# Performance work log

Measured on AMD Instinct MI355X. Metric: run time of the kernel, lower is better.

## Reference

```python
import jax, jax.numpy as jnp
import numpy as np

N_DETS = 8192
DEG = 64
E = N_DETS * DEG
NUM_BLOCKS = 8
SHORTCUT = 128   # shortcutDim
RED = 32         # reducedDim
INNER = 64       # blockInnerDim = 2*32
PW_RAW = 9
PW_HID = 256
PW_OUT = 32


def setup_inputs() -> dict:
    key = jax.random.key(0)
    ks = jax.random.split(key, 24)
    # valid boxes: x2 > x1, y2 > y1
    x1 = jax.random.uniform(ks[0], (N_DETS, 1), jnp.float32, 0.0, 1000.0)
    y1 = jax.random.uniform(ks[1], (N_DETS, 1), jnp.float32, 0.0, 1000.0)
    w = jax.random.uniform(ks[2], (N_DETS, 1), jnp.float32, 8.0, 128.0)
    h = jax.random.uniform(ks[3], (N_DETS, 1), jnp.float32, 8.0, 128.0)
    dtBoxes = jnp.concatenate([x1, y1, x1 + w, y1 + h], axis=1)
    detScores = jax.random.uniform(ks[4], (N_DETS, 1), jnp.float32)
    # every detection has DEG neighbors (first one is itself) -> no empty segments
    cIdxs = jnp.repeat(jnp.arange(N_DETS, dtype=jnp.int32), DEG)
    nIdxs = jax.random.randint(ks[5], (E,), 0, N_DETS, dtype=jnp.int32)
    nIdxs = nIdxs.at[::DEG].set(jnp.arange(N_DETS, dtype=jnp.int32))
    detFeatures = jnp.zeros((N_DETS, SHORTCUT), jnp.float32)

    def lin(k, fan_in, fan_out):
        b = 1.0 / np.sqrt(fan_in)
        return jax.random.uniform(k, (fan_in, fan_out), jnp.float32, -b, b)

    inp = dict(detScores=detScores, dtBoxes=dtBoxes, detFeatures=detFeatures,
               cIdxs=cIdxs, nIdxs=nIdxs)
    # pairwise feature generator MLP: 9 -> 256 -> 256 -> 32 (ReLU after each)
    inp['pw_W0'] = lin(ks[6], PW_RAW, PW_HID); inp['pw_b0'] = jnp.zeros((PW_HID,), jnp.float32)
    inp['pw_W1'] = lin(ks[7], PW_HID, PW_HID); inp['pw_b1'] = jnp.zeros((PW_HID,), jnp.float32)
    inp['pw_W2'] = lin(ks[8], PW_HID, PW_OUT); inp['pw_b2'] = jnp.zeros((PW_OUT,), jnp.float32)
    # per-block params, stacked over NUM_BLOCKS
    B = NUM_BLOCKS
    inp['blk_fc1_W'] = jnp.stack([lin(jax.random.fold_in(ks[9], i), SHORTCUT, RED) for i in range(B)])
    inp['blk_fc1_b'] = jnp.zeros((B, RED), jnp.float32)
    inp['blk_pw1_W'] = jnp.stack([lin(jax.random.fold_in(ks[10], i), 3 * RED, INNER) for i in range(B)])
    inp['blk_pw1_b'] = jnp.zeros((B, INNER), jnp.float32)
    inp['blk_pw2_W'] = jnp.stack([lin(jax.random.fold_in(ks[11], i), INNER, INNER) for i in range(B)])
    inp['blk_pw2_b'] = jnp.zeros((B, INNER), jnp.float32)
    inp['blk_post_W'] = jnp.stack([jnp.stack([lin(jax.random.fold_in(ks[12], 2 * i + j), INNER, INNER) for j in range(2)]) for i in range(B)])
    inp['blk_post_b'] = jnp.zeros((B, 2, INNER), jnp.float32)
    inp['blk_out_W'] = jnp.stack([lin(jax.random.fold_in(ks[13], i), INNER, SHORTCUT) for i in range(B)])
    inp['blk_out_b'] = jnp.zeros((B, SHORTCUT), jnp.float32)
    return inp


def _pairwise_raw(detScores, dtBoxes, cIdxs, nIdxs):
    # box data (getBoxData)
    x1, y1, x2, y2 = (dtBoxes[:, i:i + 1] for i in range(4))
    w, h = x2 - x1, y2 - y1
    area = w * h
    c, n = cIdxs, nIdxs
    # per-edge IoU (dt_dt_iou gathered at (c,n))
    ix = jnp.maximum(0.0, jnp.minimum(x2[c], x2[n]) - jnp.maximum(x1[c], x1[n]))
    iy = jnp.maximum(0.0, jnp.minimum(y2[c], y2[n]) - jnp.maximum(y1[c], y1[n]))
    inter = ix * iy
    iou = inter / (area[c] + area[n] - inter)
    c_w, c_h, n_w, n_h = w[c], h[c], w[n], h[n]
    c_scale = (c_w + c_h) / 2.0
    c_cx, c_cy = x1[c] + c_w / 2.0, y1[c] + c_h / 2.0
    n_cx, n_cy = x1[n] + n_w / 2.0, y1[n] + n_h / 2.0
    x_dist = n_cx - c_cx
    y_dist = n_cy - c_cy
    l2_dist = jnp.sqrt(x_dist ** 2 + y_dist ** 2) / c_scale
    x_dist = x_dist / c_scale
    y_dist = y_dist / c_scale
    log2 = jnp.log(jnp.float32(2.0))
    w_diff = jnp.log(n_w / c_w) / log2
    h_diff = jnp.log(n_h / c_h) / log2
    aspect_diff = (jnp.log(n_w / n_h) - jnp.log(c_w / c_h)) / log2
    return jnp.concatenate([detScores[c], detScores[n], iou, x_dist, y_dist,
                            l2_dist, w_diff, h_diff, aspect_diff], axis=1)  # [E,9]


def reference(detScores, dtBoxes, detFeatures, pw_W0, pw_b0, pw_W1, pw_b1,
              pw_W2, pw_b2, blk_fc1_W, blk_fc1_b, blk_pw1_W, blk_pw1_b,
              blk_pw2_W, blk_pw2_b, blk_post_W, blk_post_b, blk_out_W,
              blk_out_b, cIdxs, nIdxs):
    relu = jax.nn.relu
    numDets = detFeatures.shape[0]
    raw = _pairwise_raw(detScores, dtBoxes, cIdxs, nIdxs)
    pf = relu(raw @ pw_W0 + pw_b0)
    pf = relu(pf @ pw_W1 + pw_b1)
    pairFeatures = relu(pf @ pw_W2 + pw_b2)  # [E,32]

    f = detFeatures
    for i in range(blk_fc1_W.shape[0]):
        f1 = relu(f @ blk_fc1_W[i] + blk_fc1_b[i])                       # [N,32]
        comb = jnp.concatenate([pairFeatures, f1[cIdxs], f1[nIdxs]], 1)  # [E,96]
        comb = relu(comb @ blk_pw1_W[i] + blk_pw1_b[i])
        comb = relu(comb @ blk_pw2_W[i] + blk_pw2_b[i])                  # [E,64]
        pooled = jax.ops.segment_max(comb, cIdxs, num_segments=numDets)  # [N,64]
        pooled = relu(pooled @ blk_post_W[i, 0] + blk_post_b[i, 0])
        pooled = relu(pooled @ blk_post_W[i, 1] + blk_post_b[i, 1])
        f = relu(f + pooled @ blk_out_W[i] + blk_out_b[i])               # [N,128]
    return f
```

## Files before the change

### kernel.cpp

```cpp
#include <hip/hip_runtime.h>
#include <hip/hip_bf16.h>

typedef _Float16 half8 __attribute__((ext_vector_type(8)));
typedef __fp16 fp16x2 __attribute__((ext_vector_type(2)));
typedef float f32x4 __attribute__((ext_vector_type(4)));

#define N_DETS 8192

#define OFF_W0P   0
#define OFF_W1P   8192
#define OFF_W2P   73728
#define OFF_FC1P  81920
#define OFF_PW1P  114688
#define OFF_PW2P  163840
#define OFF_POSTP 196608
#define OFF_OUTP  262144
#define OFF_F1A   327680
#define OFF_F1B   589824
#define OFF_PFP   1114112
#define OFF_FBUF_BYTES 35782656


__device__ inline f32x4 mfma16(half8 a, half8 b, f32x4 c){
  return __builtin_amdgcn_mfma_f32_16x16x32_f16(a, b, c, 0, 0, 0);
}
__device__ inline half8 ldg8(const _Float16* p){ return *(const half8*)p; }

__device__ inline unsigned pkrtz(float a, float b){
  union { fp16x2 h; unsigned u; } x;
  x.h = __builtin_amdgcn_cvt_pkrtz(a, b);
  return x.u;
}
__device__ inline unsigned hmax2u(unsigned a, unsigned b){
  unsigned r;
  asm("v_pk_max_f16 %0, %1, %2" : "=v"(r) : "v"(a), "v"(b));
  return r;
}
__device__ inline unsigned hadd2u(unsigned a, unsigned b){
  unsigned r;
  asm("v_pk_add_f16 %0, %1, %2" : "=v"(r) : "v"(a), "v"(b));
  return r;
}

__device__ inline half8 cvtpack(f32x4 A, f32x4 B){
  union { unsigned w[4]; half8 h; } r;
  r.w[0] = pkrtz(A[0], A[1]); r.w[1] = pkrtz(A[2], A[3]);
  r.w[2] = pkrtz(B[0], B[1]); r.w[3] = pkrtz(B[2], B[3]);
  return r.h;
}
__device__ inline half8 cvtpackbr(f32x4 A, f32x4 B, const unsigned* pb){
  union { unsigned w[4]; half8 h; } r;
  r.w[0] = pkrtz(A[0], A[1]); r.w[1] = pkrtz(A[2], A[3]);
  r.w[2] = pkrtz(B[0], B[1]); r.w[3] = pkrtz(B[2], B[3]);
#pragma unroll
  for (int i = 0; i < 4; ++i) r.w[i] = hmax2u(hadd2u(r.w[i], pb[i]), 0u);
  return r.h;
}
__device__ inline half8 cvtpackr(f32x4 A, f32x4 B){
  union { unsigned w[4]; half8 h; } r;
  r.w[0] = pkrtz(A[0], A[1]); r.w[1] = pkrtz(A[2], A[3]);
  r.w[2] = pkrtz(B[0], B[1]); r.w[3] = pkrtz(B[2], B[3]);
#pragma unroll
  for (int i = 0; i < 4; ++i) r.w[i] = hmax2u(r.w[i], 0u);
  return r.h;
}

__device__ inline void packB(const float* W, int Ksrc, int Nn, _Float16* dst, int sig){
  int ns = (Ksrc + 31) >> 5;
  int t = sig / (ns * 64);
  int rem = sig - t * ns * 64;
  int s = rem >> 6;
  int l = rem & 63;
  int col = t * 16 + (l & 15);
  int g = l >> 4;
  half8 v;
#pragma unroll
  for (int j = 0; j < 8; ++j){
    int k = s*32 + ((j>>2)<<4) + g*4 + (j&3);
    v[j] = (_Float16)((k < Ksrc) ? W[k * Nn + col] : 0.f);
  }
  *(half8*)(dst + sig * 8) = v;
}

__device__ inline void packW0(const float* W, const float* bias, _Float16* dst, int sig){
  int t = sig >> 6, l = sig & 63;
  int col = t * 16 + (l & 15);
  int g = l >> 4;
  half8 v;
#pragma unroll
  for (int j = 0; j < 8; ++j){
    int k = ((j>>2)<<4) + g*4 + (j&3);
    float x = 0.f;
    if (k < 9) x = W[k * 256 + col];
    else if (k == 9) x = bias[col];
    v[j] = (_Float16)x;
  }
  *(half8*)(dst + sig * 8) = v;
}

__global__ __launch_bounds__(256) void kPrep(const float* pwW0, const float* pwb0,
    const float* pwW1, const float* pwW2,
    const float* fc1W, const float* pw1W, const float* pw2W, const float* postW, const float* outW,
    _Float16* wsh){
  int sig = blockIdx.x * 256 + threadIdx.x;
  if (sig < 1024){ packW0(pwW0, pwb0, wsh + OFF_W0P, sig); return; }
  sig -= 1024;
  if (sig < 8192){ packB(pwW1, 256, 256, wsh + OFF_W1P, sig); return; }
  sig -= 8192;
  if (sig < 1024){ packB(pwW2, 256, 32, wsh + OFF_W2P, sig); return; }
  sig -= 1024;
  int i = sig / 3840;
  int q = sig - i * 3840;
  if (q < 512){ packB(fc1W + i*4096, 128, 32, wsh + OFF_FC1P + i*4096, q); return; }
  q -= 512;
  if (q < 768){ packB(pw1W + i*6144, 96, 64, wsh + OFF_PW1P + i*6144, q); return; }
  q -= 768;
  if (q < 512){ packB(pw2W + i*4096, 64, 64, wsh + OFF_PW2P + i*4096, q); return; }
  q -= 512;
  if (q < 512){ packB(postW + i*8192, 64, 64, wsh + OFF_POSTP + i*8192, q); return; }
  q -= 512;
  if (q < 512){ packB(postW + i*8192 + 4096, 64, 64, wsh + OFF_POSTP + i*8192 + 4096, q); return; }
  q -= 512;
  packB(outW + i*8192, 64, 128, wsh + OFF_OUTP + i*8192, q);
}

__global__ __launch_bounds__(256) void kP(const float* scores, const float* boxes,
    const int* cI, const int* nI, const float* b1, const float* b2,
    const _Float16* W0p, const _Float16* W1p, const _Float16* W2p, _Float16* pfp){
  __shared__ __align__(16) _Float16 sbuf[2][8192];
  __shared__ __align__(16) _Float16 rawp[4096];
  int tid = threadIdx.x;
  int lane = tid & 63, wave = tid >> 6;
  const f32x4 fz = {0.f, 0.f, 0.f, 0.f};

  half8 w0ld[4], s0ld[4];
#pragma unroll
  for (int it = 0; it < 4; ++it){
    w0ld[it] = ldg8(W0p + it*2048 + tid*8);
    s0ld[it] = ldg8(W1p + it*2048 + tid*8);
  }
  {
    half8 z = {0,0,0,0,0,0,0,0};
#pragma unroll
    for (int it = 0; it < 2; ++it) *(half8*)(rawp + it*2048 + tid*8) = z;
  }
  __syncthreads();
  if (tid < 128){
    int e = blockIdx.x*128 + tid;
    int c = cI[e], n = nI[e];
    float cx1 = boxes[c*4+0], cy1 = boxes[c*4+1], cx2 = boxes[c*4+2], cy2 = boxes[c*4+3];
    float nx1 = boxes[n*4+0], ny1 = boxes[n*4+1], nx2 = boxes[n*4+2], ny2 = boxes[n*4+3];
    float cw = cx2-cx1, ch = cy2-cy1, nw = nx2-nx1, nh = ny2-ny1;
    float ca = cw*ch, na = nw*nh;
    float ix = fmaxf(fminf(cx2,nx2) - fmaxf(cx1,nx1), 0.f);
    float iy = fmaxf(fminf(cy2,ny2) - fmaxf(cy1,ny1), 0.f);
    float inter = ix*iy;
    float iou = inter / (ca + na - inter);
    float cs = (cw + ch) * 0.5f;
    float xd = (nx1 + nw*0.5f) - (cx1 + cw*0.5f);
    float yd = (ny1 + nh*0.5f) - (cy1 + ch*0.5f);
    float l2 = sqrtf(xd*xd + yd*yd) / cs;
    float wd = log2f(nw/cw), hd = log2f(nh/ch);
    float ad = log2f(nw/nh) - log2f(cw/ch);
    float rv[10] = {scores[c], scores[n], iou, xd/cs, yd/cs, l2, wd, hd, ad, 1.0f};
    int base = (tid >> 4) * 512;
    int r = tid & 15;
#pragma unroll
    for (int k = 0; k < 10; ++k)
      rawp[base + (((k>>2)&3)*16 + r)*8 + (k&3)] = (_Float16)rv[k];
  }
#pragma unroll
  for (int it = 0; it < 4; ++it){
    *(half8*)(&sbuf[0][0] + it*2048 + tid*8) = w0ld[it];
    *(half8*)(&sbuf[1][0] + it*2048 + tid*8) = s0ld[it];
  }
  __syncthreads();

  half8 h0f[2][8];
#pragma unroll
  for (int et = 0; et < 2; ++et){
    half8 braw = *(const half8*)(rawp + ((wave*2+et)*64 + lane)*8);
#pragma unroll
    for (int mp = 0; mp < 8; ++mp){
      f32x4 a = mfma16(*(const half8*)(&sbuf[0][0] + (2*mp)*512   + lane*8), braw, fz);
      f32x4 b = mfma16(*(const half8*)(&sbuf[0][0] + (2*mp+1)*512 + lane*8), braw, fz);
      h0f[et][mp] = cvtpackr(a, b);
    }
  }
  __syncthreads();

  int q = lane >> 4;
  f32x4 apf[2][2];
  apf[0][0] = fz; apf[0][1] = fz; apf[1][0] = fz; apf[1][1] = fz;
  for (int mp = 0; mp < 8; ++mp){
    const _Float16* cur = &sbuf[(mp+1)&1][0];
    half8 stg[4];
    if (mp < 7){
#pragma unroll
      for (int it = 0; it < 4; ++it)
        stg[it] = ldg8(W1p + (mp+1)*8192 + it*2048 + tid*8);
    }
    f32x4 acc[2][2];
    acc[0][0] = fz; acc[0][1] = fz; acc[1][0] = fz; acc[1][1] = fz;
#pragma unroll
    for (int s = 0; s < 8; ++s){
      half8 A0 = *(const half8*)(cur + s*512       + lane*8);
      half8 A1 = *(const half8*)(cur + (8+s)*512   + lane*8);
#pragma unroll
      for (int et = 0; et < 2; ++et){
        acc[et][0] = mfma16(A0, h0f[et][s], acc[et][0]);
        acc[et][1] = mfma16(A1, h0f[et][s], acc[et][1]);
      }
    }
    unsigned pb[4];
    pb[0] = pkrtz(b1[mp*32 + q*4 + 0], b1[mp*32 + q*4 + 1]);
    pb[1] = pkrtz(b1[mp*32 + q*4 + 2], b1[mp*32 + q*4 + 3]);
    pb[2] = pkrtz(b1[mp*32 + 16 + q*4 + 0], b1[mp*32 + 16 + q*4 + 1]);
    pb[3] = pkrtz(b1[mp*32 + 16 + q*4 + 2], b1[mp*32 + 16 + q*4 + 3]);
    half8 w2a = ldg8(W2p + mp*512 + lane*8);
    half8 w2b = ldg8(W2p + (8+mp)*512 + lane*8);
#pragma unroll
    for (int et = 0; et < 2; ++et){
      half8 h1f = cvtpackbr(acc[et][0], acc[et][1], pb);
      apf[et][0] = mfma16(w2a, h1f, apf[et][0]);
      apf[et][1] = mfma16(w2b, h1f, apf[et][1]);
    }
    if (mp < 7){
      _Float16* nxt = &sbuf[mp&1][0];
#pragma unroll
      for (int it = 0; it < 4; ++it)
        *(half8*)(nxt + it*2048 + tid*8) = stg[it];
    }
    __syncthreads();
  }
  unsigned pc[4];
  pc[0] = pkrtz(b2[q*4 + 0], b2[q*4 + 1]);
  pc[1] = pkrtz(b2[q*4 + 2], b2[q*4 + 3]);
  pc[2] = pkrtz(b2[16 + q*4 + 0], b2[16 + q*4 + 1]);
  pc[3] = pkrtz(b2[16 + q*4 + 2], b2[16 + q*4 + 3]);
#pragma unroll
  for (int et = 0; et < 2; ++et){
    half8 pf = cvtpackbr(apf[et][0], apf[et][1], pc);
    *(half8*)(pfp + (blockIdx.x*8 + wave*2 + et)*512 + lane*8) = pf;
  }
}

__global__ __launch_bounds__(256) void kF1(const float* detF, const _Float16* fc1p,
    const float* fb, _Float16* f1G){
  int lane = threadIdx.x & 63, wave = threadIdx.x >> 6;
  int q = lane >> 4, e = lane & 15;
  int det = (blockIdx.x * 4 + wave) * 16 + e;
  const f32x4 fz = {0.f, 0.f, 0.f, 0.f};
  half8 ff[4];
#pragma unroll
  for (int s = 0; s < 4; ++s){
    const float* p = detF + det*128 + s*32 + q*4;
    f32x4 x0 = *(const f32x4*)(p);
    f32x4 x1 = *(const f32x4*)(p + 16);
    union { unsigned w[4]; half8 h; } u;
    u.w[0] = pkrtz(x0[0], x0[1]); u.w[1] = pkrtz(x0[2], x0[3]);
    u.w[2] = pkrtz(x1[0], x1[1]); u.w[3] = pkrtz(x1[2], x1[3]);
    ff[s] = u.h;
  }
#pragma unroll
  for (int m = 0; m < 2; ++m){
    f32x4 a = fz;
#pragma unroll
    for (int s = 0; s < 4; ++s)
      a = mfma16(ldg8(fc1p + (m*4+s)*512 + lane*8), ff[s], a);
    f32x4 bv = *(const f32x4*)(fb + m*16 + q*4);
    unsigned u0 = pkrtz(fmaxf(a[0]+bv[0],0.f), fmaxf(a[1]+bv[1],0.f));
    unsigned u1 = pkrtz(fmaxf(a[2]+bv[2],0.f), fmaxf(a[3]+bv[3],0.f));
    *(unsigned*)(f1G + det*32 + q*8 + m*4)     = u0;
    *(unsigned*)(f1G + det*32 + q*8 + m*4 + 2) = u1;
  }
}

__global__ __launch_bounds__(256) void kBlk(const _Float16* pfp, const _Float16* f1in,
    _Float16* f1out, const int* nI, const _Float16* pw1p, const _Float16* pw2p,
    const _Float16* post0p, const _Float16* post1p, const _Float16* outp, const _Float16* fc1pn,
    const float* bb1, const float* bb2, const float* pb0, const float* pb1, const float* ob,
    const float* fbn, const float* fin, float* fout, int doF1){
  __shared__ __align__(16) _Float16 poolS[1024];
  int tid = threadIdx.x, lane = tid & 63, wave = tid >> 6;
  int q = lane >> 4, e = lane & 15;
  int base = blockIdx.x * 16;
  const f32x4 fz = {0.f, 0.f, 0.f, 0.f};

  half8 aW1[4][3], aW2[4][2];
  f32x4 b1v[4];
  unsigned b2p[8];
#pragma unroll
  for (int m = 0; m < 4; ++m){
#pragma unroll
    for (int k = 0; k < 3; ++k) aW1[m][k] = ldg8(pw1p + (m*3+k)*512 + lane*8);
#pragma unroll
    for (int k = 0; k < 2; ++k) aW2[m][k] = ldg8(pw2p + (m*2+k)*512 + lane*8);
    b1v[m] = *(const f32x4*)(bb1 + m*16 + q*4);
    b2p[m*2+0] = pkrtz(bb2[m*16 + q*4 + 0], bb2[m*16 + q*4 + 1]);
    b2p[m*2+1] = pkrtz(bb2[m*16 + q*4 + 2], bb2[m*16 + q*4 + 3]);
  }

  for (int dd = 0; dd < 4; ++dd){
    int d = wave*4 + dd;
    int det = base + d;
    half8 Bc = ldg8(f1in + det*32 + q*8);
    int nn[4];
#pragma unroll
    for (int et = 0; et < 4; ++et) nn[et] = nI[det*64 + et*16 + e];
    half8 Bpf[4], Bn[4];
#pragma unroll
    for (int et = 0; et < 4; ++et){
      Bpf[et] = ldg8(pfp + (det*4+et)*512 + lane*8);
      Bn[et]  = ldg8(f1in + nn[et]*32 + q*8);
    }
    f32x4 bcb[4];
#pragma unroll
    for (int m = 0; m < 4; ++m){
      f32x4 dc = mfma16(aW1[m][1], Bc, fz);
#pragma unroll
      for (int r = 0; r < 4; ++r) bcb[m][r] = dc[r] + b1v[m][r];
    }
    unsigned pm[8];
#pragma unroll
    for (int i = 0; i < 8; ++i) pm[i] = 0xFC00FC00u;
#pragma unroll
    for (int et = 0; et < 4; ++et){
      f32x4 acc[4];
#pragma unroll
      for (int m = 0; m < 4; ++m){
        acc[m] = mfma16(aW1[m][0], Bpf[et], fz);
        acc[m] = mfma16(aW1[m][2], Bn[et], acc[m]);
      }
      f32x4 r0, r1, r2, r3;
#pragma unroll
      for (int r = 0; r < 4; ++r){
        r0[r] = fmaxf(acc[0][r] + bcb[0][r], 0.f);
        r1[r] = fmaxf(acc[1][r] + bcb[1][r], 0.f);
        r2[r] = fmaxf(acc[2][r] + bcb[2][r], 0.f);
        r3[r] = fmaxf(acc[3][r] + bcb[3][r], 0.f);
      }
      half8 h1a = cvtpack(r0, r1);
      half8 h1b = cvtpack(r2, r3);
      f32x4 a2[4];
#pragma unroll
      for (int m = 0; m < 4; ++m){
        a2[m] = mfma16(aW2[m][0], h1a, fz);
        a2[m] = mfma16(aW2[m][1], h1b, a2[m]);
      }
      union { half8 h; unsigned w[4]; } uA, uB;
      uA.h = cvtpack(a2[0], a2[1]);
      uB.h = cvtpack(a2[2], a2[3]);
#pragma unroll
      for (int i = 0; i < 4; ++i){
        pm[i]   = hmax2u(pm[i],   uA.w[i]);
        pm[4+i] = hmax2u(pm[4+i], uB.w[i]);
      }
    }
#pragma unroll
    for (int s = 1; s <= 8; s <<= 1){
#pragma unroll
      for (int i = 0; i < 8; ++i)
        pm[i] = hmax2u(pm[i], __shfl_xor(pm[i], s));
    }
#pragma unroll
    for (int i = 0; i < 8; ++i)
      pm[i] = hmax2u(hadd2u(pm[i], b2p[i]), 0u);
    if (e == 0){
      union { unsigned w[4]; half8 h; } o0, o1;
#pragma unroll
      for (int i = 0; i < 4; ++i){ o0.w[i] = pm[i]; o1.w[i] = pm[4+i]; }
      *(half8*)(poolS + d*32 + q*8)       = o0.h;
      *(half8*)(poolS + 512 + d*32 + q*8) = o1.h;
    }
  }
  __syncthreads();

  half8 Bp0 = *(const half8*)(poolS + e*32 + q*8);
  half8 Bp1 = *(const half8*)(poolS + 512 + e*32 + q*8);
  int det = base + e;
  f32x4 t0[4];
#pragma unroll
  for (int m = 0; m < 4; ++m){
    f32x4 a = mfma16(ldg8(post0p + (m*2)*512   + lane*8), Bp0, fz);
    a = mfma16(ldg8(post0p + (m*2+1)*512 + lane*8), Bp1, a);
    f32x4 bv = *(const f32x4*)(pb0 + m*16 + q*4);
#pragma unroll
    for (int r = 0; r < 4; ++r) t0[m][r] = fmaxf(a[r] + bv[r], 0.f);
  }
  half8 p1a = cvtpack(t0[0], t0[1]);
  half8 p1b = cvtpack(t0[2], t0[3]);
#pragma unroll
  for (int m = 0; m < 4; ++m){
    f32x4 a = mfma16(ldg8(post1p + (m*2)*512   + lane*8), p1a, fz);
    a = mfma16(ldg8(post1p + (m*2+1)*512 + lane*8), p1b, a);
    f32x4 bv = *(const f32x4*)(pb1 + m*16 + q*4);
#pragma unroll
    for (int r = 0; r < 4; ++r) t0[m][r] = fmaxf(a[r] + bv[r], 0.f);
  }
  half8 p2a = cvtpack(t0[0], t0[1]);
  half8 p2b = cvtpack(t0[2], t0[3]);
  f32x4 fr[8];
#pragma unroll
  for (int m = 0; m < 8; ++m){
    f32x4 a = mfma16(ldg8(outp + (m*2)*512   + lane*8), p2a, fz);
    a = mfma16(ldg8(outp + (m*2+1)*512 + lane*8), p2b, a);
    f32x4 bv = *(const f32x4*)(ob + m*16 + q*4);
    f32x4 fv = *(const f32x4*)(fin + det*128 + m*16 + q*4);
#pragma unroll
    for (int r = 0; r < 4; ++r) fr[m][r] = fmaxf(fv[r] + a[r] + bv[r], 0.f);
  }
#pragma unroll
  for (int mm = 0; mm < 2; ++mm){
    int m = wave*2 + mm;
    *(f32x4*)(fout + det*128 + m*16 + q*4) = fr[m];
  }
  if (doF1 && wave == 0){
    half8 ff[4];
#pragma unroll
    for (int s = 0; s < 4; ++s) ff[s] = cvtpack(fr[2*s], fr[2*s+1]);
#pragma unroll
    for (int m = 0; m < 2; ++m){
      f32x4 a = fz;
#pragma unroll
      for (int s = 0; s < 4; ++s)
        a = mfma16(ldg8(fc1pn + (m*4+s)*512 + lane*8), ff[s], a);
      f32x4 bv = *(const f32x4*)(fbn + m*16 + q*4);
      unsigned u0 = pkrtz(fmaxf(a[0]+bv[0],0.f), fmaxf(a[1]+bv[1],0.f));
      unsigned u1 = pkrtz(fmaxf(a[2]+bv[2],0.f), fmaxf(a[3]+bv[3],0.f));
      *(unsigned*)(f1out + det*32 + q*8 + m*4)     = u0;
      *(unsigned*)(f1out + det*32 + q*8 + m*4 + 2) = u1;
    }
  }
}

extern "C" void kernel_launch(void* const* d_in, const int* in_sizes, int n_in,
                              void* d_out, int out_size, void* d_ws, size_t ws_size,
                              hipStream_t stream){
  const float* detScores   = (const float*)d_in[0];
  const float* dtBoxes     = (const float*)d_in[1];
  const float* detFeatures = (const float*)d_in[2];
  const int*   cI          = (const int*)d_in[3];
  const int*   nI          = (const int*)d_in[4];
  const float* pwW0 = (const float*)d_in[5];
  const float* pwb0 = (const float*)d_in[6];
  const float* pwW1 = (const float*)d_in[7];
  const float* pwb1 = (const float*)d_in[8];
  const float* pwW2 = (const float*)d_in[9];
  const float* pwb2 = (const float*)d_in[10];
  const float* fc1W = (const float*)d_in[11];
  const float* fc1b = (const float*)d_in[12];
  const float* pw1W = (const float*)d_in[13];
  const float* pw1b = (const float*)d_in[14];
  const float* pw2W = (const float*)d_in[15];
  const float* pw2b = (const float*)d_in[16];
  const float* postW = (const float*)d_in[17];
  const float* postb = (const float*)d_in[18];
  const float* outW  = (const float*)d_in[19];
  const float* outb  = (const float*)d_in[20];

  _Float16* wsh  = (_Float16*)d_ws;
  float*    fbuf = (float*)((char*)d_ws + OFF_FBUF_BYTES);
  _Float16* f1A  = wsh + OFF_F1A;
  _Float16* f1B  = wsh + OFF_F1B;
  _Float16* pfp  = wsh + OFF_PFP;

  kPrep<<<160, 256, 0, stream>>>(pwW0, pwb0, pwW1, pwW2, fc1W, pw1W, pw2W, postW, outW, wsh);
  kF1<<<128, 256, 0, stream>>>(detFeatures, wsh + OFF_FC1P, fc1b, f1A);
  kP<<<4096, 256, 0, stream>>>(detScores, dtBoxes, cI, nI, pwb1, pwb2,
      wsh + OFF_W0P, wsh + OFF_W1P, wsh + OFF_W2P, pfp);

  for (int i = 0; i < 8; ++i){
    int last = (i == 7);
    _Float16* fin1  = (i & 1) ? f1B : f1A;
    _Float16* fout1 = (i & 1) ? f1A : f1B;
    kBlk<<<512, 256, 0, stream>>>(pfp, fin1, fout1, nI,
        wsh + OFF_PW1P + i*6144, wsh + OFF_PW2P + i*4096,
        wsh + OFF_POSTP + i*8192, wsh + OFF_POSTP + i*8192 + 4096, wsh + OFF_OUTP + i*8192,
        wsh + OFF_FC1P + ((i+1) & 7)*4096,
        pw1b + i*64, pw2b + i*64, postb + i*128, postb + i*128 + 64, outb + i*128,
        fc1b + ((i+1) & 7)*32,
        (i == 0) ? detFeatures : fbuf, last ? (float*)d_out : fbuf, last ? 0 : 1);
  }
}
```

Baseline: 283.5 us.

## Double edges per pairwise-MLP block, remap kBlk block order, split output projection

The pairwise MLP kernel now handles 256 edges per block instead of 128, with each wave carrying four edge tiles. This amortizes the per-block streaming of the W1 weights through shared memory over twice as many MFMAs and halves the grid size. The cost is more registers, so launch bounds are set to two blocks. Separately, kBlk remaps block indices to interleave detection ranges, probably for cache or XCD locality. Its output projection now computes all eight column tiles only in wave 0, which also feeds the next block's fc1, while the other waves compute just their own two tiles, removing redundant MFMAs.

```diff
diff --git a/kernel.cpp b/kernel.cpp
--- a/kernel.cpp
+++ b/kernel.cpp
@@ -124,11 +124,11 @@
   packB(outW + i*8192, 64, 128, wsh + OFF_OUTP + i*8192, q);
 }
 
-__global__ __launch_bounds__(256) void kP(const float* scores, const float* boxes,
+__global__ __launch_bounds__(256, 2) void kP(const float* scores, const float* boxes,
     const int* cI, const int* nI, const float* b1, const float* b2,
     const _Float16* W0p, const _Float16* W1p, const _Float16* W2p, _Float16* pfp){
   __shared__ __align__(16) _Float16 sbuf[2][8192];
-  __shared__ __align__(16) _Float16 rawp[4096];
+  __shared__ __align__(16) _Float16 rawp[8192];
   int tid = threadIdx.x;
   int lane = tid & 63, wave = tid >> 6;
   const f32x4 fz = {0.f, 0.f, 0.f, 0.f};
@@ -142,11 +142,11 @@
   {
     half8 z = {0,0,0,0,0,0,0,0};
 #pragma unroll
-    for (int it = 0; it < 2; ++it) *(half8*)(rawp + it*2048 + tid*8) = z;
+    for (int it = 0; it < 4; ++it) *(half8*)(rawp + it*2048 + tid*8) = z;
   }
   __syncthreads();
-  if (tid < 128){
-    int e = blockIdx.x*128 + tid;
+  {
+    int e = blockIdx.x*256 + tid;
     int c = cI[e], n = nI[e];
     float cx1 = boxes[c*4+0], cy1 = boxes[c*4+1], cx2 = boxes[c*4+2], cy2 = boxes[c*4+3];
     float nx1 = boxes[n*4+0], ny1 = boxes[n*4+1], nx2 = boxes[n*4+2], ny2 = boxes[n*4+3];
@@ -176,22 +176,30 @@
   }
   __syncthreads();
 
-  half8 h0f[2][8];
-#pragma unroll
-  for (int et = 0; et < 2; ++et){
-    half8 braw = *(const half8*)(rawp + ((wave*2+et)*64 + lane)*8);
+  half8 h0f[4][8];
+  {
+    half8 braw[4];
+#pragma unroll
+    for (int et = 0; et < 4; ++et)
+      braw[et] = *(const half8*)(rawp + ((wave*4+et)*64 + lane)*8);
 #pragma unroll
     for (int mp = 0; mp < 8; ++mp){
-      f32x4 a = mfma16(*(const half8*)(&sbuf[0][0] + (2*mp)*512   + lane*8), braw, fz);
-      f32x4 b = mfma16(*(const half8*)(&sbuf[0][0] + (2*mp+1)*512 + lane*8), braw, fz);
-      h0f[et][mp] = cvtpackr(a, b);
+      half8 A0 = *(const half8*)(&sbuf[0][0] + (2*mp)*512   + lane*8);
+      half8 A1 = *(const half8*)(&sbuf[0][0] + (2*mp+1)*512 + lane*8);
+#pragma unroll
+      for (int et = 0; et < 4; ++et){
+        f32x4 a = mfma16(A0, braw[et], fz);
+        f32x4 b = mfma16(A1, braw[et], fz);
+        h0f[et][mp] = cvtpackr(a, b);
+      }
     }
   }
   __syncthreads();
 
   int q = lane >> 4;
-  f32x4 apf[2][2];
-  apf[0][0] = fz; apf[0][1] = fz; apf[1][0] = fz; apf[1][1] = fz;
+  f32x4 apf[4][2];
+#pragma unroll
+  for (int et = 0; et < 4; ++et){ apf[et][0] = fz; apf[et][1] = fz; }
   for (int mp = 0; mp < 8; ++mp){
     const _Float16* cur = &sbuf[(mp+1)&1][0];
     half8 stg[4];
@@ -200,14 +208,15 @@
       for (int it = 0; it < 4; ++it)
         stg[it] = ldg8(W1p + (mp+1)*8192 + it*2048 + tid*8);
     }
-    f32x4 acc[2][2];
-    acc[0][0] = fz; acc[0][1] = fz; acc[1][0] = fz; acc[1][1] = fz;
+    f32x4 acc[4][2];
+#pragma unroll
+    for (int et = 0; et < 4; ++et){ acc[et][0] = fz; acc[et][1] = fz; }
 #pragma unroll
     for (int s = 0; s < 8; ++s){
       half8 A0 = *(const half8*)(cur + s*512       + lane*8);
       half8 A1 = *(const half8*)(cur + (8+s)*512   + lane*8);
 #pragma unroll
-      for (int et = 0; et < 2; ++et){
+      for (int et = 0; et < 4; ++et){
         acc[et][0] = mfma16(A0, h0f[et][s], acc[et][0]);
         acc[et][1] = mfma16(A1, h0f[et][s], acc[et][1]);
       }
@@ -220,7 +229,7 @@
     half8 w2a = ldg8(W2p + mp*512 + lane*8);
     half8 w2b = ldg8(W2p + (8+mp)*512 + lane*8);
 #pragma unroll
-    for (int et = 0; et < 2; ++et){
+    for (int et = 0; et < 4; ++et){
       half8 h1f = cvtpackbr(acc[et][0], acc[et][1], pb);
       apf[et][0] = mfma16(w2a, h1f, apf[et][0]);
       apf[et][1] = mfma16(w2b, h1f, apf[et][1]);
@@ -239,9 +248,9 @@
   pc[2] = pkrtz(b2[16 + q*4 + 0], b2[16 + q*4 + 1]);
   pc[3] = pkrtz(b2[16 + q*4 + 2], b2[16 + q*4 + 3]);
 #pragma unroll
-  for (int et = 0; et < 2; ++et){
+  for (int et = 0; et < 4; ++et){
     half8 pf = cvtpackbr(apf[et][0], apf[et][1], pc);
-    *(half8*)(pfp + (blockIdx.x*8 + wave*2 + et)*512 + lane*8) = pf;
+    *(half8*)(pfp + (blockIdx.x*16 + wave*4 + et)*512 + lane*8) = pf;
   }
 }
 
@@ -284,7 +293,8 @@
   __shared__ __align__(16) _Float16 poolS[1024];
   int tid = threadIdx.x, lane = tid & 63, wave = tid >> 6;
   int q = lane >> 4, e = lane & 15;
-  int base = blockIdx.x * 16;
+  int bid = blockIdx.x;
+  int base = ((bid & 7) * 64 + (bid >> 3)) * 16;
   const f32x4 fz = {0.f, 0.f, 0.f, 0.f};
 
   half8 aW1[4][3], aW2[4][2];
@@ -400,36 +410,48 @@
   }
   half8 p2a = cvtpack(t0[0], t0[1]);
   half8 p2b = cvtpack(t0[2], t0[3]);
-  f32x4 fr[8];
-#pragma unroll
-  for (int m = 0; m < 8; ++m){
-    f32x4 a = mfma16(ldg8(outp + (m*2)*512   + lane*8), p2a, fz);
-    a = mfma16(ldg8(outp + (m*2+1)*512 + lane*8), p2b, a);
-    f32x4 bv = *(const f32x4*)(ob + m*16 + q*4);
-    f32x4 fv = *(const f32x4*)(fin + det*128 + m*16 + q*4);
-#pragma unroll
-    for (int r = 0; r < 4; ++r) fr[m][r] = fmaxf(fv[r] + a[r] + bv[r], 0.f);
-  }
-#pragma unroll
-  for (int mm = 0; mm < 2; ++mm){
-    int m = wave*2 + mm;
-    *(f32x4*)(fout + det*128 + m*16 + q*4) = fr[m];
-  }
-  if (doF1 && wave == 0){
-    half8 ff[4];
-#pragma unroll
-    for (int s = 0; s < 4; ++s) ff[s] = cvtpack(fr[2*s], fr[2*s+1]);
-#pragma unroll
-    for (int m = 0; m < 2; ++m){
-      f32x4 a = fz;
-#pragma unroll
-      for (int s = 0; s < 4; ++s)
-        a = mfma16(ldg8(fc1pn + (m*4+s)*512 + lane*8), ff[s], a);
-      f32x4 bv = *(const f32x4*)(fbn + m*16 + q*4);
-      unsigned u0 = pkrtz(fmaxf(a[0]+bv[0],0.f), fmaxf(a[1]+bv[1],0.f));
-      unsigned u1 = pkrtz(fmaxf(a[2]+bv[2],0.f), fmaxf(a[3]+bv[3],0.f));
-      *(unsigned*)(f1out + det*32 + q*8 + m*4)     = u0;
-      *(unsigned*)(f1out + det*32 + q*8 + m*4 + 2) = u1;
+  if (wave == 0){
+    f32x4 fr[8];
+#pragma unroll
+    for (int m = 0; m < 8; ++m){
+      f32x4 a = mfma16(ldg8(outp + (m*2)*512   + lane*8), p2a, fz);
+      a = mfma16(ldg8(outp + (m*2+1)*512 + lane*8), p2b, a);
+      f32x4 bv = *(const f32x4*)(ob + m*16 + q*4);
+      f32x4 fv = *(const f32x4*)(fin + det*128 + m*16 + q*4);
+#pragma unroll
+      for (int r = 0; r < 4; ++r) fr[m][r] = fmaxf(fv[r] + a[r] + bv[r], 0.f);
+    }
+    *(f32x4*)(fout + det*128 + 0*16 + q*4) = fr[0];
+    *(f32x4*)(fout + det*128 + 1*16 + q*4) = fr[1];
+    if (doF1){
+      half8 ff[4];
+#pragma unroll
+      for (int s = 0; s < 4; ++s) ff[s] = cvtpack(fr[2*s], fr[2*s+1]);
+#pragma unroll
+      for (int m = 0; m < 2; ++m){
+        f32x4 a = fz;
+#pragma unroll
+        for (int s = 0; s < 4; ++s)
+          a = mfma16(ldg8(fc1pn + (m*4+s)*512 + lane*8), ff[s], a);
+        f32x4 bv = *(const f32x4*)(fbn + m*16 + q*4);
+        unsigned u0 = pkrtz(fmaxf(a[0]+bv[0],0.f), fmaxf(a[1]+bv[1],0.f));
+        unsigned u1 = pkrtz(fmaxf(a[2]+bv[2],0.f), fmaxf(a[3]+bv[3],0.f));
+        *(unsigned*)(f1out + det*32 + q*8 + m*4)     = u0;
+        *(unsigned*)(f1out + det*32 + q*8 + m*4 + 2) = u1;
+      }
+    }
+  } else {
+#pragma unroll
+    for (int mm = 0; mm < 2; ++mm){
+      int m = wave*2 + mm;
+      f32x4 a = mfma16(ldg8(outp + (m*2)*512   + lane*8), p2a, fz);
+      a = mfma16(ldg8(outp + (m*2+1)*512 + lane*8), p2b, a);
+      f32x4 bv = *(const f32x4*)(ob + m*16 + q*4);
+      f32x4 fv = *(const f32x4*)(fin + det*128 + m*16 + q*4);
+      f32x4 fr;
+#pragma unroll
+      for (int r = 0; r < 4; ++r) fr[r] = fmaxf(fv[r] + a[r] + bv[r], 0.f);
+      *(f32x4*)(fout + det*128 + m*16 + q*4) = fr;
     }
   }
 }
@@ -467,7 +489,7 @@
 
   kPrep<<<160, 256, 0, stream>>>(pwW0, pwb0, pwW1, pwW2, fc1W, pw1W, pw2W, postW, outW, wsh);
   kF1<<<128, 256, 0, stream>>>(detFeatures, wsh + OFF_FC1P, fc1b, f1A);
-  kP<<<4096, 256, 0, stream>>>(detScores, dtBoxes, cI, nI, pwb1, pwb2,
+  kP<<<2048, 256, 0, stream>>>(detScores, dtBoxes, cI, nI, pwb1, pwb2,
       wsh + OFF_W0P, wsh + OFF_W1P, wsh + OFF_W2P, pfp);
 
   for (int i = 0; i < 8; ++i){
```

Result: faster. 241.9 us (-14.7%).
